# Kernel optimization log

Hardware: AMD Instinct MI355X
Metric: run time of the kernel (lower is better)

## Reference

```python
import jax, jax.numpy as jnp
import numpy as np
from jax import lax

B, T, K = 64, 2048, 128


def setup_inputs() -> dict:
    key = jax.random.key(0)
    k0, k1, k2, k3, k4, k5 = jax.random.split(key, 6)
    emissions = jax.random.normal(k0, (B, T, K), dtype=jnp.float32)
    lengths = jax.random.randint(k1, (B,), T // 2, T + 1)
    mask = jnp.arange(T)[None, :] < lengths[:, None]  # left-aligned [B,T] bool
    target = jax.random.bernoulli(k2, 0.5, (B, T, K))  # supervision set [B,T,K] bool
    forbidden_transitions = jax.random.bernoulli(k3, 0.1, (K, K))
    transitions = jax.random.normal(k4, (K, K), dtype=jnp.float32) * 0.01
    start_transitions = jax.random.normal(k5, (K,), dtype=jnp.float32) * 0.01
    return dict(emissions=emissions, mask=mask, target=target,
                transitions=transitions, start_transitions=start_transitions,
                forbidden_transitions=forbidden_transitions)


def reference(emissions, mask, target, transitions, start_transitions, forbidden_transitions):
    # Faithful to torch forward: transitions masked with -10000; end_transitions unused;
    # raw (unmasked) start_transitions added to EVERY timestep (as in the source).
    trans = jnp.where(forbidden_transitions, jnp.float32(-10000.0), transitions)  # [K,K]
    sup_em = jnp.where(target, emissions, jnp.float32(-100000.0))  # masked_fill(~target)
    bi = jnp.concatenate([sup_em, emissions], axis=0)  # [2B,T,K]
    bi = bi + start_transitions  # broadcast over all timesteps (source quirk)

    alpha0 = bi[:, 0]  # [2B,K]

    def step(alpha, em_t):
        # logdotexp: logsumexp_i(alpha[:,i] + trans[i,j]) + em_t[:,j]
        new = jax.nn.logsumexp(alpha[:, :, None] + trans[None, :, :], axis=1) + em_t
        return new, new

    _, outs = lax.scan(step, alpha0, jnp.swapaxes(bi[:, 1:], 0, 1))  # [T-1,2B,K]
    outs = jnp.concatenate([alpha0[None], outs], axis=0)  # [T,2B,K]

    lengths = mask.sum(-1)  # [B]
    last = jnp.concatenate([lengths, lengths]) - 1  # [2B]
    z_alpha = outs[last, jnp.arange(2 * B)]  # alpha at last valid step, [2B,K]
    z = jax.nn.logsumexp(z_alpha, axis=-1)  # [2B]
    supervised_z = z[:B]
    unsupervised_z = z[B:]
    return supervised_z - unsupervised_z
```

## Files before the change

kernel.cpp:

```cpp
#include <hip/hip_runtime.h>
#include <stdint.h>

#define BB 64
#define TT 2048
#define KK 128
#define CH 32
#define WSTRIDE 132

typedef float f32x16 __attribute__((ext_vector_type(16)));
typedef float f32x2  __attribute__((ext_vector_type(2)));

__device__ __forceinline__ float waveMax(float v) {
#pragma unroll
    for (int off = 32; off; off >>= 1) v = fmaxf(v, __shfl_xor(v, off, 64));
    return v;
}
__device__ __forceinline__ float waveSum(float v) {
#pragma unroll
    for (int off = 32; off; off >>= 1) v += __shfl_xor(v, off, 64);
    return v;
}
__device__ __forceinline__ int waveSumI(int v) {
#pragma unroll
    for (int off = 32; off; off >>= 1) v += __shfl_xor(v, off, 64);
    return v;
}
__device__ __forceinline__ float quadSum(float s) {
    int x = __builtin_amdgcn_mov_dpp(__float_as_int(s), 0xB1, 0xf, 0xf, true);
    s += __int_as_float(x);
    x = __builtin_amdgcn_mov_dpp(__float_as_int(s), 0x4E, 0xf, 0xf, true);
    s += __int_as_float(x);
    return s;
}
__device__ __forceinline__ float waveMaxFast(float v) {
    int x = __builtin_amdgcn_mov_dpp(__float_as_int(v), 0xB1, 0xf, 0xf, true);
    v = fmaxf(v, __int_as_float(x));
    x = __builtin_amdgcn_mov_dpp(__float_as_int(v), 0x4E, 0xf, 0xf, true);
    v = fmaxf(v, __int_as_float(x));
#pragma unroll
    for (int off = 4; off <= 32; off <<= 1) v = fmaxf(v, __shfl_xor(v, off, 64));
    return v;
}

template<int C> __device__ __forceinline__ float dppMax(float v) {
    int x = __builtin_amdgcn_mov_dpp(__float_as_int(v), C, 0xf, 0xf, true);
    return fmaxf(v, __int_as_float(x));
}
__device__ __forceinline__ float waveMaxTo63(float v) {
    v = dppMax<0xB1>(v);
    v = dppMax<0x4E>(v);
    v = dppMax<0x124>(v);
    v = dppMax<0x128>(v);
    v = dppMax<0x142>(v);
    v = dppMax<0x143>(v);
    return v;
}

__device__ __forceinline__ void lds_barrier() {
    asm volatile("s_waitcnt lgkmcnt(0)\n\ts_barrier" ::: "memory");
}

#define PKFMA(ep, wp, acc) acc = __builtin_elementwise_fma(ep, wp, acc)

#define MATVEC_QUARTER(Wa, Wb, ev, sOut) {                          \
    const float4 e0 = ev[0], e1 = ev[1], e2 = ev[2], e3 = ev[3];    \
    const float4 e4 = ev[4], e5 = ev[5], e6 = ev[6], e7 = ev[7];    \
    f32x2 a0 = {0.f,0.f}, a1 = {0.f,0.f}, a2 = {0.f,0.f}, a3 = {0.f,0.f}; \
    PKFMA(((f32x2){e0.x, e0.y}), ((f32x2){Wa[0],  Wa[1]}),  a0);    \
    PKFMA(((f32x2){e0.z, e0.w}), ((f32x2){Wa[2],  Wa[3]}),  a1);    \
    PKFMA(((f32x2){e1.x, e1.y}), ((f32x2){Wa[4],  Wa[5]}),  a2);    \
    PKFMA(((f32x2){e1.z, e1.w}), ((f32x2){Wa[6],  Wa[7]}),  a3);    \
    PKFMA(((f32x2){e2.x, e2.y}), ((f32x2){Wa[8],  Wa[9]}),  a0);    \
    PKFMA(((f32x2){e2.z, e2.w}), ((f32x2){Wa[10], Wa[11]}), a1);    \
    PKFMA(((f32x2){e3.x, e3.y}), ((f32x2){Wa[12], Wa[13]}), a2);    \
    PKFMA(((f32x2){e3.z, e3.w}), ((f32x2){Wa[14], Wa[15]}), a3);    \
    PKFMA(((f32x2){e4.x, e4.y}), ((f32x2){Wb[0],  Wb[1]}),  a0);    \
    PKFMA(((f32x2){e4.z, e4.w}), ((f32x2){Wb[2],  Wb[3]}),  a1);    \
    PKFMA(((f32x2){e5.x, e5.y}), ((f32x2){Wb[4],  Wb[5]}),  a2);    \
    PKFMA(((f32x2){e5.z, e5.w}), ((f32x2){Wb[6],  Wb[7]}),  a3);    \
    PKFMA(((f32x2){e6.x, e6.y}), ((f32x2){Wb[8],  Wb[9]}),  a0);    \
    PKFMA(((f32x2){e6.z, e6.w}), ((f32x2){Wb[10], Wb[11]}), a1);    \
    PKFMA(((f32x2){e7.x, e7.y}), ((f32x2){Wb[12], Wb[13]}), a2);    \
    PKFMA(((f32x2){e7.z, e7.w}), ((f32x2){Wb[14], Wb[15]}), a3);    \
    const f32x2 s2 = (a0 + a1) + (a2 + a3);                         \
    sOut = s2[0] + s2[1]; }

extern "C" __global__ __launch_bounds__(128, 1)
void crf_fb_kernel(const float* __restrict__ em,
                   const int* __restrict__ mask,
                   const int* __restrict__ tgt,
                   const float* __restrict__ trans,
                   const float* __restrict__ start,
                   const int* __restrict__ forb,
                   float* __restrict__ ef,
                   float* __restrict__ db,
                   float* __restrict__ Mfb)
{
    const int tid  = threadIdx.x;
    const int k    = tid;
    const int w    = tid >> 6;
    const int lane = tid & 63;
    const bool fwdDir = (blockIdx.x < 2 * BB);
    const int c    = blockIdx.x & (2 * BB - 1);
    const int b    = c & (BB - 1);
    const bool sup = (c < BB);

    extern __shared__ __align__(16) float Wlds[];
    __shared__ __align__(16) float biLDS[2][CH][KK];
    __shared__ __align__(16) float eLDS[2][KK];
    __shared__ __align__(8)  float wmLDS[2];
    __shared__ float redLDS[2];
    __shared__ int lenLDS;

    if (tid == 0) lenLDS = 0;
    int ps = 0;
    const int4* __restrict__ mrow = (const int4*)(mask + (size_t)b * TT);
#pragma unroll
    for (int it = 0; it < 4; ++it) {
        const int4 m4 = mrow[tid + 128 * it];
        ps += m4.x + m4.y + m4.z + m4.w;
    }
    ps = waveSumI(ps);
    __syncthreads();
    if (lane == 0) atomicAdd(&lenLDS, ps);

    const float st = start[k];
    const float* __restrict__ emrow = em + (size_t)b * TT * KK;
    const int* __restrict__ trow = tgt + (size_t)b * TT * KK;

#pragma unroll 4
    for (int r = 0; r < KK; ++r) {
        const float tv = trans[r * KK + tid];
        const int   fv = forb [r * KK + tid];
        const float wv = fv ? 0.0f : __expf(tv);
        const int   R  = fwdDir ? tid : r;
        const int   i  = fwdDir ? r   : tid;
        Wlds[R * WSTRIDE + i] = wv;
    }
    __syncthreads();
    const int len = lenLDS;
    const int mid = len >> 1;
    const int N   = fwdDir ? mid : (len - 1 - mid);
    const int t0  = fwdDir ? 0 : (len - 1);

    float v0 = emrow[(size_t)t0 * KK + k];
    if (sup && !trow[(size_t)t0 * KK + k]) v0 = -100000.0f;
    v0 += st;
    const float wm0 = waveMax(v0);
    if (lane == 0) redLDS[w] = wm0;
    __syncthreads();
    const float M0 = fmaxf(redLDS[0], redLDS[1]);
    double M = (double)M0;
    float eNew = __expf(v0 - M0);
    eLDS[0][k] = eNew;

    const int scol = (tid & 31) << 2;
    const float4 stc = *(const float4*)(start + scol);
    auto stageChunk = [&](int bf, int m) {
        const int base_n = 1 + CH * m;
        const int t_base = fwdDir ? base_n : (len - base_n - CH);
#pragma unroll
        for (int i = 0; i < 8; ++i) {
            const int row = (tid >> 5) + (i << 2);
            const int t = t_base + row;
            float4 e4 = *(const float4*)(emrow + (size_t)t * KK + scol);
            if (sup) {
                const int4 t4 = *(const int4*)(trow + (size_t)t * KK + scol);
                e4.x = t4.x ? e4.x : -100000.0f;
                e4.y = t4.y ? e4.y : -100000.0f;
                e4.z = t4.z ? e4.z : -100000.0f;
                e4.w = t4.w ? e4.w : -100000.0f;
            }
            e4.x += stc.x; e4.y += stc.y; e4.z += stc.z; e4.w += stc.w;
            *(float4*)&biLDS[bf][row][scol] = e4;
        }
    };

    const int nChunks = (N + CH - 1) / CH;
    int buf = 0;
    stageChunk(0, 0);
    const float* __restrict__ Wrow = &Wlds[k * WSTRIDE];
    lds_barrier();

    for (int m = 0; m < nChunks; ++m) {
        if (m + 1 < nChunks) stageChunk(buf ^ 1, m + 1);
        const int base_n = 1 + CH * m;
        const int rem = N - base_n + 1;
        const int lim = rem < CH ? rem : CH;
#pragma unroll 4
        for (int i = 0; i < lim; ++i) {
            const int n = base_n + i;
            const int p = (n - 1) & 1;

            const int pos = fwdDir ? i : (CH - 1 - i);
            float bi = biLDS[buf][pos][k];
            if (!fwdDir && n == N) bi = 0.0f;

            if ((n & 3) == 3) {
                const float u = waveMaxTo63(__logf(eNew));
                if (lane == 63) wmLDS[w] = u;
            }
            float r = 0.0f;
            if ((n & 3) == 0) {
                const float2 wmv = *(const float2*)wmLDS;
                r = fmaxf(wmv.x, wmv.y);
                M += (double)r;
            }
            const float f = __expf(bi - r);

            const float4* __restrict__ ev = (const float4*)eLDS[p];
            const float4* __restrict__ wv4 = (const float4*)Wrow;
            f32x2 a0 = {0.f,0.f}, a1 = {0.f,0.f}, a2 = {0.f,0.f}, a3 = {0.f,0.f};
#pragma unroll
            for (int j = 0; j < 32; j += 4) {
                const float4 W0 = wv4[j], W1 = wv4[j + 1], W2 = wv4[j + 2], W3 = wv4[j + 3];
                const float4 E0 = ev[j], E1 = ev[j + 1], E2 = ev[j + 2], E3 = ev[j + 3];
                PKFMA(((f32x2){E0.x, E0.y}), ((f32x2){W0.x, W0.y}), a0);
                PKFMA(((f32x2){E0.z, E0.w}), ((f32x2){W0.z, W0.w}), a1);
                PKFMA(((f32x2){E1.x, E1.y}), ((f32x2){W1.x, W1.y}), a2);
                PKFMA(((f32x2){E1.z, E1.w}), ((f32x2){W1.z, W1.w}), a3);
                PKFMA(((f32x2){E2.x, E2.y}), ((f32x2){W2.x, W2.y}), a0);
                PKFMA(((f32x2){E2.z, E2.w}), ((f32x2){W2.z, W2.w}), a1);
                PKFMA(((f32x2){E3.x, E3.y}), ((f32x2){W3.x, W3.y}), a2);
                PKFMA(((f32x2){E3.z, E3.w}), ((f32x2){W3.z, W3.w}), a3);
            }
            const f32x2 aa = (a0 + a1) + (a2 + a3);
            const float s = aa[0] + aa[1];

            eNew = s * f;
            eLDS[p ^ 1][k] = eNew;

            lds_barrier();
        }
        buf ^= 1;
    }

    (fwdDir ? ef : db)[(size_t)c * KK + k] = eNew;
    if (tid == 0) Mfb[(fwdDir ? 0 : 2 * BB) + c] = (float)M;
}

extern "C" __global__ void crf_combine_kernel(const float* __restrict__ ef,
                                              const float* __restrict__ db,
                                              const float* __restrict__ Mfb,
                                              float* __restrict__ out)
{
    const int b = blockIdx.x;
    const int tid = threadIdx.x;
    const int wv = tid >> 6, lane = tid & 63;
    __shared__ float red[2][2];
    __shared__ float z[2];
#pragma unroll
    for (int s = 0; s < 2; ++s) {
        const int c = b + s * BB;
        const float v = ef[(size_t)c * KK + tid] * db[(size_t)c * KK + tid];
        const float p = waveSum(v);
        if (lane == 0) red[s][wv] = p;
    }
    __syncthreads();
    if (tid < 2) {
        const int c = b + tid * BB;
        z[tid] = Mfb[c] + Mfb[2 * BB + c] + __logf(red[tid][0] + red[tid][1]);
    }
    __syncthreads();
    if (tid == 0) out[b] = z[0] - z[1];
}

extern "C" __global__ __launch_bounds__(512)
__attribute__((amdgpu_waves_per_eu(2, 2)))
void crf_chain_kernel(const float* __restrict__ em, const int* __restrict__ mask,
                      const int* __restrict__ tgt, const float* __restrict__ trans,
                      const float* __restrict__ start, const int* __restrict__ forb,
                      float* __restrict__ zbuf)
{
    const int tid = threadIdx.x;
    const int k = tid >> 2, q = tid & 3, w = tid >> 6, lane = tid & 63;
    const int c = blockIdx.x, b = c & (BB - 1);
    const bool sup = (c < BB);
    __shared__ __align__(16) float eLDS[2][KK];
    __shared__ float wmLDS[8];
    __shared__ float redLDS[8];
    __shared__ int lenLDS;
    if (tid == 0) lenLDS = 0;
    const int4 m4 = ((const int4*)(mask + (size_t)b * TT))[tid];
    int ps = m4.x + m4.y + m4.z + m4.w;
    ps = waveSumI(ps);
    __syncthreads();
    if (lane == 0) atomicAdd(&lenLDS, ps);
    const float st = start[k];
    const float* __restrict__ emrow = em + (size_t)b * TT * KK;
    const int* __restrict__ trow = tgt + (size_t)b * TT * KK;
    const int ib = q * 32;
    f32x16 Wa, Wb;
#pragma unroll
    for (int j = 0; j < 16; ++j) {
        Wa[j] = forb[(ib + j     ) * KK + k] ? 0.0f : __expf(trans[(ib + j     ) * KK + k]);
        Wb[j] = forb[(ib + 16 + j) * KK + k] ? 0.0f : __expf(trans[(ib + 16 + j) * KK + k]);
    }
    float v0 = emrow[k];
    if (sup && !trow[k]) v0 = -100000.0f;
    v0 += st;
    const float wm0 = waveMax(v0);
    if (lane == 0) redLDS[w] = wm0;
    __syncthreads();
    const int len = lenLDS;
    float M0 = fmaxf(fmaxf(fmaxf(redLDS[0], redLDS[1]), fmaxf(redLDS[2], redLDS[3])),
                     fmaxf(fmaxf(redLDS[4], redLDS[5]), fmaxf(redLDS[6], redLDS[7])));
    double M = (double)M0;
    float eNew = __expf(v0 - M0);
    if (q == 0) eLDS[0][k] = eNew;
    auto bival = [&](int t) -> float {
        float e0 = emrow[(size_t)t * KK + k];
        if (sup) { if (!trow[(size_t)t * KK + k]) e0 = -100000.0f; }
        return e0 + st;
    };
    float biA = (len > 1) ? bival(1) : 0.0f;
    float biB = (len > 2) ? bival(2) : 0.0f;
    float biC = (len > 3) ? bival(3) : 0.0f;
    float biD = (len > 4) ? bival(4) : 0.0f;
    float sPrev = 1.0f, baPrev = 0.0f;
    lds_barrier();
#pragma unroll 4
    for (int t = 1; t < len; ++t) {
        const int p = (t - 1) & 1;
        const float biN = (t + 4 < len) ? bival(t + 4) : 0.0f;
        if ((t & 3) == 3) {
            const float u = __logf(sPrev) + baPrev;
            const float wmx = waveMaxFast(u);
            if (lane == 0) wmLDS[w] = wmx;
        }
        float r = 0.0f;
        if ((t & 3) == 0) {
            r = fmaxf(fmaxf(fmaxf(wmLDS[0], wmLDS[1]), fmaxf(wmLDS[2], wmLDS[3])),
                      fmaxf(fmaxf(wmLDS[4], wmLDS[5]), fmaxf(wmLDS[6], wmLDS[7])));
            M += (double)r;
        }
        const float ba = biA - r;
        const float f = __expf(ba);
        const float4* __restrict__ ev = (const float4*)eLDS[p] + q * 8;
        float s;
        MATVEC_QUARTER(Wa, Wb, ev, s)
        s = quadSum(s);
        eNew = s * f;
        if (q == 0) eLDS[p ^ 1][k] = eNew;
        sPrev = s; baPrev = ba;
        biA = biB; biB = biC; biC = biD; biD = biN;
        lds_barrier();
    }
    const float sm = waveSum((q == 0) ? eNew : 0.0f);
    if (lane == 0) redLDS[w] = sm;
    __syncthreads();
    if (tid == 0) {
        const float ss = ((redLDS[0] + redLDS[1]) + (redLDS[2] + redLDS[3]))
                       + ((redLDS[4] + redLDS[5]) + (redLDS[6] + redLDS[7]));
        zbuf[c] = (float)(M + (double)__logf(ss));
    }
}

extern "C" __global__ void crf_final_kernel(const float* __restrict__ z,
                                            float* __restrict__ out)
{
    const int b = threadIdx.x;
    out[b] = z[b] - z[b + BB];
}

extern "C" void kernel_launch(void* const* d_in, const int* in_sizes, int n_in,
                              void* d_out, int out_size, void* d_ws, size_t ws_size,
                              hipStream_t stream) {
    const float* em    = (const float*)d_in[0];
    const int*   mask  = (const int*)d_in[1];
    const int*   tgt   = (const int*)d_in[2];
    const float* trans = (const float*)d_in[3];
    const float* start = (const float*)d_in[4];
    const int*   forb  = (const int*)d_in[5];

    const size_t need = (size_t)(2 * 2 * BB * KK + 4 * BB) * sizeof(float);
    if (ws_size >= need) {
        float* ef  = (float*)d_ws;
        float* db  = ef + 2 * BB * KK;
        float* Mfb = db + 2 * BB * KK;
        const size_t wbytes = (size_t)KK * WSTRIDE * sizeof(float);
        crf_fb_kernel<<<4 * BB, 128, wbytes, stream>>>(em, mask, tgt, trans, start,
                                                       forb, ef, db, Mfb);
        crf_combine_kernel<<<BB, 128, 0, stream>>>(ef, db, Mfb, (float*)d_out);
    } else {
        float* zbuf = (float*)d_ws;
        crf_chain_kernel<<<2 * BB, 512, 0, stream>>>(em, mask, tgt, trans, start,
                                                     forb, zbuf);
        crf_final_kernel<<<1, BB, 0, stream>>>(zbuf, (float*)d_out);
    }
}
```

Baseline: 938.0 us.

## Run forward-backward CRF chain with one wave per block, two states per lane

Each forward and backward chain block now uses a single 64-lane wave, and every lane computes two output states. This removes the per-timestep workgroup barrier and the cross-wave max exchange through LDS. Both are replaced by a wave-local LDS wait and a register-held pending rescale value. The transition matrix is stored in LDS in an interleaved layout so each lane reads its two rows as float4s. The cost is twice the FMA work per lane on the serial critical path and fewer waves to hide latency.

```diff
diff --git a/kernel.cpp b/kernel.cpp
--- a/kernel.cpp
+++ b/kernel.cpp
@@ -4,8 +4,9 @@
 #define BB 64
 #define TT 2048
 #define KK 128
+#define HF 64
 #define CH 32
-#define WSTRIDE 132
+#define WSTR 260
 
 typedef float f32x16 __attribute__((ext_vector_type(16)));
 typedef float f32x2  __attribute__((ext_vector_type(2)));
@@ -24,13 +25,6 @@
 #pragma unroll
     for (int off = 32; off; off >>= 1) v += __shfl_xor(v, off, 64);
     return v;
-}
-__device__ __forceinline__ float quadSum(float s) {
-    int x = __builtin_amdgcn_mov_dpp(__float_as_int(s), 0xB1, 0xf, 0xf, true);
-    s += __int_as_float(x);
-    x = __builtin_amdgcn_mov_dpp(__float_as_int(s), 0x4E, 0xf, 0xf, true);
-    s += __int_as_float(x);
-    return s;
 }
 __device__ __forceinline__ float waveMaxFast(float v) {
     int x = __builtin_amdgcn_mov_dpp(__float_as_int(v), 0xB1, 0xf, 0xf, true);
@@ -42,20 +36,9 @@
     return v;
 }
 
-template<int C> __device__ __forceinline__ float dppMax(float v) {
-    int x = __builtin_amdgcn_mov_dpp(__float_as_int(v), C, 0xf, 0xf, true);
-    return fmaxf(v, __int_as_float(x));
-}
-__device__ __forceinline__ float waveMaxTo63(float v) {
-    v = dppMax<0xB1>(v);
-    v = dppMax<0x4E>(v);
-    v = dppMax<0x124>(v);
-    v = dppMax<0x128>(v);
-    v = dppMax<0x142>(v);
-    v = dppMax<0x143>(v);
-    return v;
-}
-
+__device__ __forceinline__ void wave_lds_fence() {
+    asm volatile("s_waitcnt lgkmcnt(0)" ::: "memory");
+}
 __device__ __forceinline__ void lds_barrier() {
     asm volatile("s_waitcnt lgkmcnt(0)\n\ts_barrier" ::: "memory");
 }
@@ -85,7 +68,7 @@
     const f32x2 s2 = (a0 + a1) + (a2 + a3);                         \
     sOut = s2[0] + s2[1]; }
 
-extern "C" __global__ __launch_bounds__(128, 1)
+extern "C" __global__ __launch_bounds__(64, 1)
 void crf_fb_kernel(const float* __restrict__ em,
                    const int* __restrict__ mask,
                    const int* __restrict__ tgt,
@@ -96,10 +79,7 @@
                    float* __restrict__ db,
                    float* __restrict__ Mfb)
 {
-    const int tid  = threadIdx.x;
-    const int k    = tid;
-    const int w    = tid >> 6;
-    const int lane = tid & 63;
+    const int k    = threadIdx.x;
     const bool fwdDir = (blockIdx.x < 2 * BB);
     const int c    = blockIdx.x & (2 * BB - 1);
     const int b    = c & (BB - 1);
@@ -107,80 +87,77 @@
 
     extern __shared__ __align__(16) float Wlds[];
     __shared__ __align__(16) float biLDS[2][CH][KK];
-    __shared__ __align__(16) float eLDS[2][KK];
-    __shared__ __align__(8)  float wmLDS[2];
-    __shared__ float redLDS[2];
-    __shared__ int lenLDS;
-
-    if (tid == 0) lenLDS = 0;
+    __shared__ __align__(16) float eLDS[2][2 * HF];
+
     int ps = 0;
     const int4* __restrict__ mrow = (const int4*)(mask + (size_t)b * TT);
 #pragma unroll
-    for (int it = 0; it < 4; ++it) {
-        const int4 m4 = mrow[tid + 128 * it];
+    for (int it = 0; it < 8; ++it) {
+        const int4 m4 = mrow[k + HF * it];
         ps += m4.x + m4.y + m4.z + m4.w;
     }
-    ps = waveSumI(ps);
-    __syncthreads();
-    if (lane == 0) atomicAdd(&lenLDS, ps);
-
-    const float st = start[k];
+    const int len = waveSumI(ps);
+
     const float* __restrict__ emrow = em + (size_t)b * TT * KK;
     const int* __restrict__ trow = tgt + (size_t)b * TT * KK;
-
+    const int col2 = k << 1;
+
+    {
 #pragma unroll 4
-    for (int r = 0; r < KK; ++r) {
-        const float tv = trans[r * KK + tid];
-        const int   fv = forb [r * KK + tid];
-        const float wv = fv ? 0.0f : __expf(tv);
-        const int   R  = fwdDir ? tid : r;
-        const int   i  = fwdDir ? r   : tid;
-        Wlds[R * WSTRIDE + i] = wv;
-    }
-    __syncthreads();
-    const int len = lenLDS;
+        for (int r = 0; r < KK; ++r) {
+            const float2 tv = *(const float2*)(trans + r * KK + col2);
+            const int2   fv = *(const int2*)  (forb  + r * KK + col2);
+            const float w0 = fv.x ? 0.0f : __expf(tv.x);
+            const float w1 = fv.y ? 0.0f : __expf(tv.y);
+            const int o0 = fwdDir ? col2     : r;
+            const int i0 = fwdDir ? r        : col2;
+            const int o1 = fwdDir ? col2 + 1 : r;
+            const int i1 = fwdDir ? r        : col2 + 1;
+            Wlds[(o0 & 63) * WSTR + ((o0 >> 6) << 7) + ((i0 & 63) << 1) + (i0 >> 6)] = w0;
+            Wlds[(o1 & 63) * WSTR + ((o1 >> 6) << 7) + ((i1 & 63) << 1) + (i1 >> 6)] = w1;
+        }
+    }
+
     const int mid = len >> 1;
     const int N   = fwdDir ? mid : (len - 1 - mid);
     const int t0  = fwdDir ? 0 : (len - 1);
 
-    float v0 = emrow[(size_t)t0 * KK + k];
-    if (sup && !trow[(size_t)t0 * KK + k]) v0 = -100000.0f;
-    v0 += st;
-    const float wm0 = waveMax(v0);
-    if (lane == 0) redLDS[w] = wm0;
-    __syncthreads();
-    const float M0 = fmaxf(redLDS[0], redLDS[1]);
+    float v0x = emrow[(size_t)t0 * KK + k];
+    float v0y = emrow[(size_t)t0 * KK + k + HF];
+    if (sup) {
+        if (!trow[(size_t)t0 * KK + k])      v0x = -100000.0f;
+        if (!trow[(size_t)t0 * KK + k + HF]) v0y = -100000.0f;
+    }
+    v0x += start[k]; v0y += start[k + HF];
+    const float M0 = waveMax(fmaxf(v0x, v0y));
     double M = (double)M0;
-    float eNew = __expf(v0 - M0);
-    eLDS[0][k] = eNew;
-
-    const int scol = (tid & 31) << 2;
-    const float4 stc = *(const float4*)(start + scol);
+    f32x2 eNew = { __expf(v0x - M0), __expf(v0y - M0) };
+    *(f32x2*)&eLDS[0][col2] = eNew;
+
+    const float2 stc = *(const float2*)(start + col2);
     auto stageChunk = [&](int bf, int m) {
         const int base_n = 1 + CH * m;
         const int t_base = fwdDir ? base_n : (len - base_n - CH);
 #pragma unroll
-        for (int i = 0; i < 8; ++i) {
-            const int row = (tid >> 5) + (i << 2);
+        for (int row = 0; row < CH; ++row) {
             const int t = t_base + row;
-            float4 e4 = *(const float4*)(emrow + (size_t)t * KK + scol);
+            float2 e2 = *(const float2*)(emrow + (size_t)t * KK + col2);
             if (sup) {
-                const int4 t4 = *(const int4*)(trow + (size_t)t * KK + scol);
-                e4.x = t4.x ? e4.x : -100000.0f;
-                e4.y = t4.y ? e4.y : -100000.0f;
-                e4.z = t4.z ? e4.z : -100000.0f;
-                e4.w = t4.w ? e4.w : -100000.0f;
+                const int2 t2 = *(const int2*)(trow + (size_t)t * KK + col2);
+                e2.x = t2.x ? e2.x : -100000.0f;
+                e2.y = t2.y ? e2.y : -100000.0f;
             }
-            e4.x += stc.x; e4.y += stc.y; e4.z += stc.z; e4.w += stc.w;
-            *(float4*)&biLDS[bf][row][scol] = e4;
+            e2.x += stc.x; e2.y += stc.y;
+            *(float2*)&biLDS[bf][row][col2] = e2;
         }
     };
 
     const int nChunks = (N + CH - 1) / CH;
     int buf = 0;
     stageChunk(0, 0);
-    const float* __restrict__ Wrow = &Wlds[k * WSTRIDE];
-    lds_barrier();
+    const float4* __restrict__ wp = (const float4*)(Wlds + k * WSTR);
+    float rPend = 0.0f;
+    wave_lds_fence();
 
     for (int m = 0; m < nChunks; ++m) {
         if (m + 1 < nChunks) stageChunk(buf ^ 1, m + 1);
@@ -191,52 +168,48 @@
         for (int i = 0; i < lim; ++i) {
             const int n = base_n + i;
             const int p = (n - 1) & 1;
-
             const int pos = fwdDir ? i : (CH - 1 - i);
-            float bi = biLDS[buf][pos][k];
-            if (!fwdDir && n == N) bi = 0.0f;
+
+            float bx = biLDS[buf][pos][k];
+            float by = biLDS[buf][pos][k + HF];
+            if (!fwdDir && n == N) { bx = 0.0f; by = 0.0f; }
 
             if ((n & 3) == 3) {
-                const float u = waveMaxTo63(__logf(eNew));
-                if (lane == 63) wmLDS[w] = u;
+                rPend = waveMaxFast(__logf(fmaxf(eNew[0], eNew[1])));
             }
             float r = 0.0f;
-            if ((n & 3) == 0) {
-                const float2 wmv = *(const float2*)wmLDS;
-                r = fmaxf(wmv.x, wmv.y);
-                M += (double)r;
+            if ((n & 3) == 0) { r = rPend; M += (double)r; }
+            const float fx = __expf(bx - r);
+            const float fy = __expf(by - r);
+
+            const float4* __restrict__ ev = (const float4*)eLDS[p];
+            f32x2 a0 = {0.f,0.f}, a0b = {0.f,0.f};
+            f32x2 a1 = {0.f,0.f}, a1b = {0.f,0.f};
+#pragma unroll 8
+            for (int cc = 0; cc < 32; ++cc) {
+                const float4 E  = ev[cc];
+                const float4 W0 = wp[cc];
+                const float4 W1 = wp[32 + cc];
+                PKFMA(((f32x2){E.x, E.y}), ((f32x2){W0.x, W0.y}), a0);
+                PKFMA(((f32x2){E.z, E.w}), ((f32x2){W0.z, W0.w}), a0b);
+                PKFMA(((f32x2){E.x, E.y}), ((f32x2){W1.x, W1.y}), a1);
+                PKFMA(((f32x2){E.z, E.w}), ((f32x2){W1.z, W1.w}), a1b);
             }
-            const float f = __expf(bi - r);
-
-            const float4* __restrict__ ev = (const float4*)eLDS[p];
-            const float4* __restrict__ wv4 = (const float4*)Wrow;
-            f32x2 a0 = {0.f,0.f}, a1 = {0.f,0.f}, a2 = {0.f,0.f}, a3 = {0.f,0.f};
-#pragma unroll
-            for (int j = 0; j < 32; j += 4) {
-                const float4 W0 = wv4[j], W1 = wv4[j + 1], W2 = wv4[j + 2], W3 = wv4[j + 3];
-                const float4 E0 = ev[j], E1 = ev[j + 1], E2 = ev[j + 2], E3 = ev[j + 3];
-                PKFMA(((f32x2){E0.x, E0.y}), ((f32x2){W0.x, W0.y}), a0);
-                PKFMA(((f32x2){E0.z, E0.w}), ((f32x2){W0.z, W0.w}), a1);
-                PKFMA(((f32x2){E1.x, E1.y}), ((f32x2){W1.x, W1.y}), a2);
-                PKFMA(((f32x2){E1.z, E1.w}), ((f32x2){W1.z, W1.w}), a3);
-                PKFMA(((f32x2){E2.x, E2.y}), ((f32x2){W2.x, W2.y}), a0);
-                PKFMA(((f32x2){E2.z, E2.w}), ((f32x2){W2.z, W2.w}), a1);
-                PKFMA(((f32x2){E3.x, E3.y}), ((f32x2){W3.x, W3.y}), a2);
-                PKFMA(((f32x2){E3.z, E3.w}), ((f32x2){W3.z, W3.w}), a3);
-            }
-            const f32x2 aa = (a0 + a1) + (a2 + a3);
-            const float s = aa[0] + aa[1];
-
-            eNew = s * f;
-            eLDS[p ^ 1][k] = eNew;
-
-            lds_barrier();
+            const f32x2 s0v = a0 + a0b;
+            const f32x2 s1v = a1 + a1b;
+            eNew[0] = (s0v[0] + s0v[1]) * fx;
+            eNew[1] = (s1v[0] + s1v[1]) * fy;
+            *(f32x2*)&eLDS[p ^ 1][col2] = eNew;
+
+            wave_lds_fence();
         }
         buf ^= 1;
     }
 
-    (fwdDir ? ef : db)[(size_t)c * KK + k] = eNew;
-    if (tid == 0) Mfb[(fwdDir ? 0 : 2 * BB) + c] = (float)M;
+    float* __restrict__ dst = (fwdDir ? ef : db) + (size_t)c * KK;
+    dst[k]      = eNew[0];
+    dst[k + HF] = eNew[1];
+    if (k == 0) Mfb[(fwdDir ? 0 : 2 * BB) + c] = (float)M;
 }
 
 extern "C" __global__ void crf_combine_kernel(const float* __restrict__ ef,
@@ -265,6 +238,22 @@
     if (tid == 0) out[b] = z[0] - z[1];
 }
 
+__device__ __forceinline__ float waveMaxFastFB(float v) {
+    int x = __builtin_amdgcn_mov_dpp(__float_as_int(v), 0xB1, 0xf, 0xf, true);
+    v = fmaxf(v, __int_as_float(x));
+    x = __builtin_amdgcn_mov_dpp(__float_as_int(v), 0x4E, 0xf, 0xf, true);
+    v = fmaxf(v, __int_as_float(x));
+#pragma unroll
+    for (int off = 4; off <= 32; off <<= 1) v = fmaxf(v, __shfl_xor(v, off, 64));
+    return v;
+}
+__device__ __forceinline__ float quadSum(float s) {
+    int x = __builtin_amdgcn_mov_dpp(__float_as_int(s), 0xB1, 0xf, 0xf, true);
+    s += __int_as_float(x);
+    x = __builtin_amdgcn_mov_dpp(__float_as_int(s), 0x4E, 0xf, 0xf, true);
+    s += __int_as_float(x);
+    return s;
+}
 extern "C" __global__ __launch_bounds__(512)
 __attribute__((amdgpu_waves_per_eu(2, 2)))
 void crf_chain_kernel(const float* __restrict__ em, const int* __restrict__ mask,
@@ -299,7 +288,9 @@
     float v0 = emrow[k];
     if (sup && !trow[k]) v0 = -100000.0f;
     v0 += st;
-    const float wm0 = waveMax(v0);
+    float wm0 = v0;
+#pragma unroll
+    for (int off = 32; off; off >>= 1) wm0 = fmaxf(wm0, __shfl_xor(wm0, off, 64));
     if (lane == 0) redLDS[w] = wm0;
     __syncthreads();
     const int len = lenLDS;
@@ -325,7 +316,7 @@
         const float biN = (t + 4 < len) ? bival(t + 4) : 0.0f;
         if ((t & 3) == 3) {
             const float u = __logf(sPrev) + baPrev;
-            const float wmx = waveMaxFast(u);
+            const float wmx = waveMaxFastFB(u);
             if (lane == 0) wmLDS[w] = wmx;
         }
         float r = 0.0f;
@@ -378,9 +369,9 @@
         float* ef  = (float*)d_ws;
         float* db  = ef + 2 * BB * KK;
         float* Mfb = db + 2 * BB * KK;
-        const size_t wbytes = (size_t)KK * WSTRIDE * sizeof(float);
-        crf_fb_kernel<<<4 * BB, 128, wbytes, stream>>>(em, mask, tgt, trans, start,
-                                                       forb, ef, db, Mfb);
+        const size_t wbytes = (size_t)HF * WSTR * sizeof(float);
+        crf_fb_kernel<<<4 * BB, 64, wbytes, stream>>>(em, mask, tgt, trans, start,
+                                                      forb, ef, db, Mfb);
         crf_combine_kernel<<<BB, 128, 0, stream>>>(ef, db, Mfb, (float*)d_out);
     } else {
         float* zbuf = (float*)d_ws;
```

After: 1.405 ms. 49.8% more time.
